# Kernel tuning notes

Measured on AMD Instinct MI355X. Metric: run time of the kernel, lower is better.

The kernel has to match this reference:

```python
import jax, jax.numpy as jnp
import numpy as np

N_NODES = 100000
N_EDGES = 3200000


def gcn_conv(x, src, dst, W, b, n):
    # x: [N, Fin] -> linear transform then symmetric-normalized scatter-add (PyG GCNConv)
    xw = x @ W  # [N, Fout]
    loop = jnp.arange(n, dtype=src.dtype)
    s = jnp.concatenate([src, loop])  # add self-loops
    d = jnp.concatenate([dst, loop])
    deg = jax.ops.segment_sum(jnp.ones_like(s, dtype=xw.dtype), d, num_segments=n)
    dinv = jnp.where(deg > 0, jax.lax.rsqrt(deg), 0.0)
    norm = dinv[s] * dinv[d]  # [E+N]
    out = jax.ops.segment_sum(xw[s] * norm[:, None], d, num_segments=n)
    return out + b


def setup_inputs() -> dict:
    key = jax.random.key(0)
    ks = jax.random.split(key, 11)
    x = jax.random.normal(ks[0], (N_NODES, 2), dtype=jnp.float32)
    edge_index = jax.random.randint(ks[1], (2, N_EDGES), 0, N_NODES, dtype=jnp.int64)
    W1 = jax.random.normal(ks[2], (2, 32), dtype=jnp.float32) * 0.5
    b1 = jax.random.normal(ks[3], (32,), dtype=jnp.float32) * 0.1
    W2 = jax.random.normal(ks[4], (32, 32), dtype=jnp.float32) * 0.18
    b2 = jax.random.normal(ks[5], (32,), dtype=jnp.float32) * 0.1
    Wf1 = jax.random.normal(ks[6], (32, 32), dtype=jnp.float32) * 0.18
    bf1 = jax.random.normal(ks[7], (32,), dtype=jnp.float32) * 0.1
    Wf2 = jax.random.normal(ks[8], (32, 1), dtype=jnp.float32) * 0.18
    bf2 = jax.random.normal(ks[9], (1,), dtype=jnp.float32) * 0.1
    return {"x": x, "edge_index": edge_index, "W1": W1, "b1": b1, "W2": W2,
            "b2": b2, "Wf1": Wf1, "bf1": bf1, "Wf2": Wf2, "bf2": bf2}


def reference(x, edge_index, W1, b1, W2, b2, Wf1, bf1, Wf2, bf2):
    n = x.shape[0]
    src, dst = edge_index[0], edge_index[1]
    h = jax.nn.relu(gcn_conv(x, src, dst, W1, b1, n))
    h = jax.nn.relu(gcn_conv(h, src, dst, W2, b2, n))
    h = jax.nn.relu(h @ Wf1 + bf1)
    return h @ Wf2 + bf2  # [N, 1]
```

## Files before the change

kernel.cpp:

```cpp
#include <hip/hip_runtime.h>

#define NGRP 512
#define CAP  6656
#define EPB  8192
#define NE   16
#define SRC_BITS 17
#define SRC_MASK 0x1FFFF

static __device__ __forceinline__ unsigned short f2bf(float f) {
    unsigned u = __float_as_uint(f);
    return (unsigned short)((u + 0x7FFFu + ((u >> 16) & 1u)) >> 16);
}
static __device__ __forceinline__ float bf2f_lo(unsigned u) { return __uint_as_float(u << 16); }
static __device__ __forceinline__ float bf2f_hi(unsigned u) { return __uint_as_float(u & 0xFFFF0000u); }


__global__ void k_init(int* gcursor) {
    gcursor[threadIdx.x] = threadIdx.x * CAP;
}

__global__ __launch_bounds__(512) void k_partition(const int* __restrict__ ei, int* gcursor,
                                                   unsigned* __restrict__ pairs,
                                                   int E, int n, int GN) {
    __shared__ int cnt[NGRP];
    __shared__ int cur[NGRP];
    int tid = threadIdx.x;
    cnt[tid] = 0;
    __syncthreads();
    int base = blockIdx.x * EPB;
    int sreg[NE], dreg[NE];
#pragma unroll
    for (int k = 0; k < NE; ++k) {
        int e = base + tid + k * 512;
        int d = -1, s = 0;
        if (e < E) {
            s = ei[e];
            d = ei[E + e];
            if ((unsigned)s < (unsigned)n && (unsigned)d < (unsigned)n)
                atomicAdd(&cnt[d / GN], 1);
            else d = -1;
        }
        sreg[k] = s; dreg[k] = d;
    }
    __syncthreads();
    { int c = cnt[tid]; cur[tid] = c ? atomicAdd(&gcursor[tid], c) : 0; }
    __syncthreads();
#pragma unroll
    for (int k = 0; k < NE; ++k) {
        int d = dreg[k];
        if (d >= 0) {
            int g = d / GN;
            int w = atomicAdd(&cur[g], 1);
            if (w < (g + 1) * CAP)
                pairs[w] = ((unsigned)(d - g * GN) << SRC_BITS) | (unsigned)sreg[k];
        }
    }
}

__global__ __launch_bounds__(512) void k_build(const int* __restrict__ gcursor,
                                               const unsigned* __restrict__ pairs,
                                               const float2* __restrict__ x2,
                                               int* __restrict__ rowStart, int* __restrict__ rowEnd,
                                               int* __restrict__ srclist, float* __restrict__ dinv,
                                               float2* __restrict__ z, int n, int GN) {
    __shared__ unsigned pl[CAP];
    __shared__ int cnt[512];
    __shared__ int cur[512];
    int g = blockIdx.x;
    int t = threadIdx.x;
    int gbeg = g * CAP;
    int gend = gcursor[g];
    int cape = gbeg + CAP;
    if (gend > cape) gend = cape;
    int m = gend - gbeg;
    cnt[t] = 0;
    __syncthreads();
    for (int k = t; k < m; k += 512) {
        unsigned v = pairs[gbeg + k];
        pl[k] = v;
        atomicAdd(&cnt[(v >> SRC_BITS) & 511], 1);
    }
    __syncthreads();
    int c = cnt[t];
    for (int off = 1; off < 512; off <<= 1) {
        int add = (t >= off) ? cnt[t - off] : 0;
        __syncthreads();
        cnt[t] += add;
        __syncthreads();
    }
    int excl = cnt[t] - c;
    int node = g * GN + t;
    if (t < GN && node < n) {
        int st = gbeg + excl;
        rowStart[node] = st;
        rowEnd[node] = st + c;
        float di = rsqrtf(1.0f + (float)c);
        dinv[node] = di;
        float2 xv = x2[node];
        z[node] = make_float2(xv.x * di, xv.y * di);
    }
    cur[t] = excl;
    __syncthreads();
    for (int k = t; k < m; k += 512) {
        unsigned v = pl[k];
        int dl = (v >> SRC_BITS) & 511;
        int pos = atomicAdd(&cur[dl], 1);
        srclist[gbeg + pos] = (int)(v & SRC_MASK);
    }
}


__global__ __launch_bounds__(256) void k_gather2f(const int* __restrict__ rowStart,
                                                  const int* __restrict__ rowEnd,
                                                  const int* __restrict__ srclist,
                                                  const float2* __restrict__ z,
                                                  float2* __restrict__ agg, int n) {
    int w = blockIdx.x * 256 + threadIdx.x;
    if (w >= n) return;
    int e = rowStart[w], end = rowEnd[w];
    float ax = 0.f, ay = 0.f;
    int s = (e < end) ? srclist[e] : 0;
    while (e < end) {
        int sc = s;
        ++e;
        if (e < end) s = srclist[e];
        float2 v = z[sc];
        ax += v.x; ay += v.y;
    }
    float2 v = z[w];
    agg[w] = make_float2(ax + v.x, ay + v.y);
}

__global__ void k_mid1(const float2* __restrict__ agg, const float* __restrict__ dinv,
                       const float* __restrict__ W1, const float* __restrict__ b1,
                       const float* __restrict__ W2, unsigned short* __restrict__ y_bf, int n) {
    __shared__ float sW[1024];
    __shared__ float sh[8][33];
    int tid = threadIdx.x;
    for (int k = tid; k < 1024; k += 256) sW[k] = W2[k];
    int ln = tid >> 5, f = tid & 31;
    int i = blockIdx.x * 8 + ln;
    float h = 0.f, di = 0.f;
    if (i < n) {
        di = dinv[i];
        float2 a = agg[i];
        h = di * (a.x * W1[f] + a.y * W1[32 + f]) + b1[f];
        h = h > 0.f ? h : 0.f;
    }
    sh[ln][f] = h;
    __syncthreads();
    if (i < n) {
        float acc = 0.f;
#pragma unroll
        for (int k = 0; k < 32; ++k) acc += sh[ln][k] * sW[k * 32 + f];
        y_bf[(size_t)i * 32 + f] = f2bf(acc * di);
    }
}

__global__ __launch_bounds__(256) void k_gather_rows(const int* __restrict__ rowStart,
                                                     const int* __restrict__ rowEnd,
                                                     const int* __restrict__ srclist,
                                                     const uint4* __restrict__ y4,
                                                     float4* __restrict__ acc4, int n) {
    int w = blockIdx.x * 64 + (threadIdx.x >> 2);
    int q = threadIdx.x & 3;
    if (w >= n) return;
    int e = rowStart[w], end = rowEnd[w];
    float a0 = 0.f, a1 = 0.f, a2 = 0.f, a3 = 0.f, a4 = 0.f, a5 = 0.f, a6 = 0.f, a7 = 0.f;
    int s = (e < end) ? srclist[e] : 0;
    while (e < end) {
        int sc = s;
        ++e;
        if (e < end) s = srclist[e];
        uint4 v = y4[(size_t)sc * 4 + q];
        a0 += bf2f_lo(v.x); a1 += bf2f_hi(v.x);
        a2 += bf2f_lo(v.y); a3 += bf2f_hi(v.y);
        a4 += bf2f_lo(v.z); a5 += bf2f_hi(v.z);
        a6 += bf2f_lo(v.w); a7 += bf2f_hi(v.w);
    }
    uint4 v = y4[(size_t)w * 4 + q];
    a0 += bf2f_lo(v.x); a1 += bf2f_hi(v.x);
    a2 += bf2f_lo(v.y); a3 += bf2f_hi(v.y);
    a4 += bf2f_lo(v.z); a5 += bf2f_hi(v.z);
    a6 += bf2f_lo(v.w); a7 += bf2f_hi(v.w);
    size_t b = (size_t)w * 8 + q * 2;
    acc4[b]     = make_float4(a0, a1, a2, a3);
    acc4[b + 1] = make_float4(a4, a5, a6, a7);
}

__global__ void k_final(const float* __restrict__ acc, const float* __restrict__ dinv,
                        const float* __restrict__ b2, const float* __restrict__ Wf1,
                        const float* __restrict__ bf1, const float* __restrict__ Wf2,
                        const float* __restrict__ bf2, float* __restrict__ out, int n) {
    __shared__ float sW[1024];
    __shared__ float sh[8][33];
    int tid = threadIdx.x;
    for (int k = tid; k < 1024; k += 256) sW[k] = Wf1[k];
    int ln = tid >> 5, f = tid & 31;
    int i = blockIdx.x * 8 + ln;
    float h = 0.f;
    if (i < n) {
        h = dinv[i] * acc[(size_t)i * 32 + f] + b2[f];
        h = h > 0.f ? h : 0.f;
    }
    sh[ln][f] = h;
    __syncthreads();
    float p = 0.f;
    if (i < n) {
        float a = bf1[f];
#pragma unroll
        for (int k = 0; k < 32; ++k) a += sh[ln][k] * sW[k * 32 + f];
        a = a > 0.f ? a : 0.f;
        p = a * Wf2[f];
    }
#pragma unroll
    for (int m = 16; m >= 1; m >>= 1) p += __shfl_xor(p, m, 64);
    if (f == 0 && i < n) out[i] = p + bf2[0];
}


extern "C" void kernel_launch(void* const* d_in, const int* in_sizes, int n_in,
                              void* d_out, int out_size, void* d_ws, size_t ws_size,
                              hipStream_t stream) {
    const float* x   = (const float*)d_in[0];
    const int*   ei  = (const int*)d_in[1];
    const float* W1  = (const float*)d_in[2];
    const float* b1  = (const float*)d_in[3];
    const float* W2  = (const float*)d_in[4];
    const float* b2  = (const float*)d_in[5];
    const float* Wf1 = (const float*)d_in[6];
    const float* bf1 = (const float*)d_in[7];
    const float* Wf2 = (const float*)d_in[8];
    const float* bf2 = (const float*)d_in[9];
    float* out = (float*)d_out;

    int n = in_sizes[0] / 2;
    int E = in_sizes[1] / 2;
    int GN = (n + NGRP - 1) / NGRP;

    float* wsf = (float*)d_ws;
    int*    srclist  = (int*)wsf;
    size_t  o = (size_t)NGRP * CAP;
    int*    rowStart = (int*)(wsf + o);     o += n;
    int*    rowEnd   = (int*)(wsf + o);     o += n;
    float*  dinv     = wsf + o;             o += n;
    float2* z        = (float2*)(wsf + o);  o += 2 * (size_t)n;
    float2* agg      = (float2*)(wsf + o);  o += 2 * (size_t)n;
    int*    gcursor  = (int*)(wsf + o);     o += NGRP;
    o = (o + 3) & ~(size_t)3;
    float*  acc      = wsf + o;             o += 32 * (size_t)n;
    unsigned short* y_bf = (unsigned short*)(wsf + o);
    unsigned* pairs = (unsigned*)acc;

    const int B = 256;
    int nblk = (E + EPB - 1) / EPB;

    k_init<<<1, NGRP, 0, stream>>>(gcursor);
    k_partition<<<nblk, 512, 0, stream>>>(ei, gcursor, pairs, E, n, GN);
    k_build<<<NGRP, 512, 0, stream>>>(gcursor, pairs, (const float2*)x, rowStart, rowEnd,
                                      srclist, dinv, z, n, GN);

    k_gather2f<<<(n + 255) / 256, B, 0, stream>>>(rowStart, rowEnd, srclist, z, agg, n);
    k_mid1<<<(n + 7) / 8, B, 0, stream>>>(agg, dinv, W1, b1, W2, y_bf, n);

    k_gather_rows<<<(n + 63) / 64, B, 0, stream>>>(rowStart, rowEnd, srclist,
                                                   (const uint4*)y_bf, (float4*)acc, n);

    k_final<<<(n + 7) / 8, B, 0, stream>>>(acc, dinv, b2, Wf1, bf1, Wf2, bf2, out, n);
}
```

Baseline: 179.8 us.

## Split layer-2 gather into two feature planes and split edges across lanes

The bf16 layer-2 features are stored as two separate 16-feature planes, each 3.2 MB rather than one 6.4 MB table, and gathered by two kernel launches so each pass's working set fits better in cache. Within a plane, each node's edge list is split between two lane pairs and the partial sums are combined with a shuffle, which gives more memory parallelism. Both gathers are also unrolled by four to issue more independent loads. In exchange, srclist and rowStart/rowEnd are read twice and there is an extra launch.

```diff
diff --git a/kernel.cpp b/kernel.cpp
--- a/kernel.cpp
+++ b/kernel.cpp
@@ -119,12 +119,14 @@
     if (w >= n) return;
     int e = rowStart[w], end = rowEnd[w];
     float ax = 0.f, ay = 0.f;
-    int s = (e < end) ? srclist[e] : 0;
-    while (e < end) {
-        int sc = s;
-        ++e;
-        if (e < end) s = srclist[e];
-        float2 v = z[sc];
+    for (; e + 4 <= end; e += 4) {
+        int s0 = srclist[e], s1 = srclist[e + 1], s2 = srclist[e + 2], s3 = srclist[e + 3];
+        float2 v0 = z[s0], v1 = z[s1], v2 = z[s2], v3 = z[s3];
+        ax += v0.x + v1.x + v2.x + v3.x;
+        ay += v0.y + v1.y + v2.y + v3.y;
+    }
+    for (; e < end; ++e) {
+        float2 v = z[srclist[e]];
         ax += v.x; ay += v.y;
     }
     float2 v = z[w];
@@ -133,7 +135,8 @@
 
 __global__ void k_mid1(const float2* __restrict__ agg, const float* __restrict__ dinv,
                        const float* __restrict__ W1, const float* __restrict__ b1,
-                       const float* __restrict__ W2, unsigned short* __restrict__ y_bf, int n) {
+                       const float* __restrict__ W2, unsigned short* __restrict__ y0,
+                       unsigned short* __restrict__ y1, int n) {
     __shared__ float sW[1024];
     __shared__ float sh[8][33];
     int tid = threadIdx.x;
@@ -153,39 +156,61 @@
         float acc = 0.f;
 #pragma unroll
         for (int k = 0; k < 32; ++k) acc += sh[ln][k] * sW[k * 32 + f];
-        y_bf[(size_t)i * 32 + f] = f2bf(acc * di);
-    }
-}
-
-__global__ __launch_bounds__(256) void k_gather_rows(const int* __restrict__ rowStart,
-                                                     const int* __restrict__ rowEnd,
-                                                     const int* __restrict__ srclist,
-                                                     const uint4* __restrict__ y4,
-                                                     float4* __restrict__ acc4, int n) {
+        unsigned short* yp = (f < 16) ? y0 : y1;
+        yp[(size_t)i * 16 + (f & 15)] = f2bf(acc * di);
+    }
+}
+
+#define ACC8(v)                                        \
+    a0 += bf2f_lo((v).x); a1 += bf2f_hi((v).x);        \
+    a2 += bf2f_lo((v).y); a3 += bf2f_hi((v).y);        \
+    a4 += bf2f_lo((v).z); a5 += bf2f_hi((v).z);        \
+    a6 += bf2f_lo((v).w); a7 += bf2f_hi((v).w);
+
+__global__ __launch_bounds__(256) void k_gather_plane(const int* __restrict__ rowStart,
+                                                      const int* __restrict__ rowEnd,
+                                                      const int* __restrict__ srclist,
+                                                      const uint4* __restrict__ yh,
+                                                      float4* __restrict__ acc4, int n, int p) {
     int w = blockIdx.x * 64 + (threadIdx.x >> 2);
-    int q = threadIdx.x & 3;
     if (w >= n) return;
-    int e = rowStart[w], end = rowEnd[w];
+    int slot = (threadIdx.x >> 1) & 1;
+    int q = threadIdx.x & 1;
+    int beg = rowStart[w], end = rowEnd[w];
+    int deg = end - beg;
+    int half = (deg + 1) >> 1;
+    int e = beg + slot * half;
+    int e1 = slot ? end : (beg + half);
     float a0 = 0.f, a1 = 0.f, a2 = 0.f, a3 = 0.f, a4 = 0.f, a5 = 0.f, a6 = 0.f, a7 = 0.f;
-    int s = (e < end) ? srclist[e] : 0;
-    while (e < end) {
-        int sc = s;
-        ++e;
-        if (e < end) s = srclist[e];
-        uint4 v = y4[(size_t)sc * 4 + q];
-        a0 += bf2f_lo(v.x); a1 += bf2f_hi(v.x);
-        a2 += bf2f_lo(v.y); a3 += bf2f_hi(v.y);
-        a4 += bf2f_lo(v.z); a5 += bf2f_hi(v.z);
-        a6 += bf2f_lo(v.w); a7 += bf2f_hi(v.w);
-    }
-    uint4 v = y4[(size_t)w * 4 + q];
-    a0 += bf2f_lo(v.x); a1 += bf2f_hi(v.x);
-    a2 += bf2f_lo(v.y); a3 += bf2f_hi(v.y);
-    a4 += bf2f_lo(v.z); a5 += bf2f_hi(v.z);
-    a6 += bf2f_lo(v.w); a7 += bf2f_hi(v.w);
-    size_t b = (size_t)w * 8 + q * 2;
-    acc4[b]     = make_float4(a0, a1, a2, a3);
-    acc4[b + 1] = make_float4(a4, a5, a6, a7);
+    for (; e + 4 <= e1; e += 4) {
+        int s0 = srclist[e], s1 = srclist[e + 1], s2 = srclist[e + 2], s3 = srclist[e + 3];
+        uint4 v0 = yh[(size_t)s0 * 2 + q];
+        uint4 v1 = yh[(size_t)s1 * 2 + q];
+        uint4 v2 = yh[(size_t)s2 * 2 + q];
+        uint4 v3 = yh[(size_t)s3 * 2 + q];
+        ACC8(v0); ACC8(v1); ACC8(v2); ACC8(v3);
+    }
+    for (; e < e1; ++e) {
+        uint4 v = yh[(size_t)srclist[e] * 2 + q];
+        ACC8(v);
+    }
+    if (slot == 0) {
+        uint4 v = yh[(size_t)w * 2 + q];
+        ACC8(v);
+    }
+    a0 += __shfl_xor(a0, 2, 64);
+    a1 += __shfl_xor(a1, 2, 64);
+    a2 += __shfl_xor(a2, 2, 64);
+    a3 += __shfl_xor(a3, 2, 64);
+    a4 += __shfl_xor(a4, 2, 64);
+    a5 += __shfl_xor(a5, 2, 64);
+    a6 += __shfl_xor(a6, 2, 64);
+    a7 += __shfl_xor(a7, 2, 64);
+    if (slot == 0) {
+        float4* dst = acc4 + (size_t)w * 8 + p * 4 + q * 2;
+        dst[0] = make_float4(a0, a1, a2, a3);
+        dst[1] = make_float4(a4, a5, a6, a7);
+    }
 }
 
 __global__ void k_final(const float* __restrict__ acc, const float* __restrict__ dinv,
@@ -249,7 +274,8 @@
     int*    gcursor  = (int*)(wsf + o);     o += NGRP;
     o = (o + 3) & ~(size_t)3;
     float*  acc      = wsf + o;             o += 32 * (size_t)n;
-    unsigned short* y_bf = (unsigned short*)(wsf + o);
+    unsigned short* y0 = (unsigned short*)(wsf + o);
+    unsigned short* y1 = y0 + (size_t)n * 16;
     unsigned* pairs = (unsigned*)acc;
 
     const int B = 256;
@@ -261,10 +287,12 @@
                                       srclist, dinv, z, n, GN);
 
     k_gather2f<<<(n + 255) / 256, B, 0, stream>>>(rowStart, rowEnd, srclist, z, agg, n);
-    k_mid1<<<(n + 7) / 8, B, 0, stream>>>(agg, dinv, W1, b1, W2, y_bf, n);
-
-    k_gather_rows<<<(n + 63) / 64, B, 0, stream>>>(rowStart, rowEnd, srclist,
-                                                   (const uint4*)y_bf, (float4*)acc, n);
+    k_mid1<<<(n + 7) / 8, B, 0, stream>>>(agg, dinv, W1, b1, W2, y0, y1, n);
+
+    k_gather_plane<<<(n + 63) / 64, B, 0, stream>>>(rowStart, rowEnd, srclist,
+                                                    (const uint4*)y0, (float4*)acc, n, 0);
+    k_gather_plane<<<(n + 63) / 64, B, 0, stream>>>(rowStart, rowEnd, srclist,
+                                                    (const uint4*)y1, (float4*)acc, n, 1);
 
     k_final<<<(n + 7) / 8, B, 0, stream>>>(acc, dinv, b2, Wf1, bf1, Wf2, bf2, out, n);
 }
```

Result: faster. 174.5 us (-2.9%).

## Replace CSR build with per-group shared-memory atomic scatter aggregation

Applied to the files above, without the earlier changes.

Drops the per-group sort into a CSR src list (rowStart/rowEnd/srclist). Degree counting and both aggregation layers now read the dst-bucketed pairs directly and accumulate into shared-memory float atomics per destination group. The second layer's 32 bf16 features are split into two 16-wide halves stored separately, each aggregated by its own launch so the shared accumulator fits. This removes the sort pass and the row-pointer indirection, but it trades register accumulation for heavy LDS atomic traffic with contention, runs only 512 blocks per launch, and adds an extra pass over the pairs.

```diff
diff --git a/kernel.cpp b/kernel.cpp
--- a/kernel.cpp
+++ b/kernel.cpp
@@ -6,6 +6,7 @@
 #define NE   16
 #define SRC_BITS 17
 #define SRC_MASK 0x1FFFF
+#define GNMAX 256
 
 static __device__ __forceinline__ unsigned short f2bf(float f) {
     unsigned u = __float_as_uint(f);
@@ -57,83 +58,60 @@
     }
 }
 
-__global__ __launch_bounds__(512) void k_build(const int* __restrict__ gcursor,
-                                               const unsigned* __restrict__ pairs,
-                                               const float2* __restrict__ x2,
-                                               int* __restrict__ rowStart, int* __restrict__ rowEnd,
-                                               int* __restrict__ srclist, float* __restrict__ dinv,
-                                               float2* __restrict__ z, int n, int GN) {
-    __shared__ unsigned pl[CAP];
+__global__ __launch_bounds__(512) void k_deg(const int* __restrict__ gcursor,
+                                             const unsigned* __restrict__ pairs,
+                                             const float2* __restrict__ x2,
+                                             float* __restrict__ dinv, float2* __restrict__ z,
+                                             int n, int GN) {
     __shared__ int cnt[512];
-    __shared__ int cur[512];
-    int g = blockIdx.x;
-    int t = threadIdx.x;
+    int g = blockIdx.x, t = threadIdx.x;
+    cnt[t] = 0;
+    __syncthreads();
     int gbeg = g * CAP;
-    int gend = gcursor[g];
-    int cape = gbeg + CAP;
-    if (gend > cape) gend = cape;
-    int m = gend - gbeg;
-    cnt[t] = 0;
-    __syncthreads();
-    for (int k = t; k < m; k += 512) {
-        unsigned v = pairs[gbeg + k];
-        pl[k] = v;
-        atomicAdd(&cnt[(v >> SRC_BITS) & 511], 1);
-    }
-    __syncthreads();
-    int c = cnt[t];
-    for (int off = 1; off < 512; off <<= 1) {
-        int add = (t >= off) ? cnt[t - off] : 0;
-        __syncthreads();
-        cnt[t] += add;
-        __syncthreads();
-    }
-    int excl = cnt[t] - c;
+    int gend = min(gcursor[g], gbeg + CAP);
+    for (int k = gbeg + t; k < gend; k += 512)
+        atomicAdd(&cnt[pairs[k] >> SRC_BITS], 1);
+    __syncthreads();
     int node = g * GN + t;
     if (t < GN && node < n) {
-        int st = gbeg + excl;
-        rowStart[node] = st;
-        rowEnd[node] = st + c;
-        float di = rsqrtf(1.0f + (float)c);
+        float di = rsqrtf(1.0f + (float)cnt[t]);
         dinv[node] = di;
         float2 xv = x2[node];
         z[node] = make_float2(xv.x * di, xv.y * di);
     }
-    cur[t] = excl;
-    __syncthreads();
-    for (int k = t; k < m; k += 512) {
-        unsigned v = pl[k];
-        int dl = (v >> SRC_BITS) & 511;
-        int pos = atomicAdd(&cur[dl], 1);
-        srclist[gbeg + pos] = (int)(v & SRC_MASK);
-    }
-}
-
-
-__global__ __launch_bounds__(256) void k_gather2f(const int* __restrict__ rowStart,
-                                                  const int* __restrict__ rowEnd,
-                                                  const int* __restrict__ srclist,
-                                                  const float2* __restrict__ z,
-                                                  float2* __restrict__ agg, int n) {
-    int w = blockIdx.x * 256 + threadIdx.x;
-    if (w >= n) return;
-    int e = rowStart[w], end = rowEnd[w];
-    float ax = 0.f, ay = 0.f;
-    int s = (e < end) ? srclist[e] : 0;
-    while (e < end) {
-        int sc = s;
-        ++e;
-        if (e < end) s = srclist[e];
-        float2 v = z[sc];
-        ax += v.x; ay += v.y;
-    }
-    float2 v = z[w];
-    agg[w] = make_float2(ax + v.x, ay + v.y);
+}
+
+
+__global__ __launch_bounds__(512) void k_gather1(const int* __restrict__ gcursor,
+                                                 const unsigned* __restrict__ pairs,
+                                                 const float2* __restrict__ z,
+                                                 float2* __restrict__ agg, int n, int GN) {
+    __shared__ float ax[512];
+    __shared__ float ay[512];
+    int g = blockIdx.x, t = threadIdx.x;
+    ax[t] = 0.f; ay[t] = 0.f;
+    __syncthreads();
+    int gbeg = g * CAP;
+    int gend = min(gcursor[g], gbeg + CAP);
+    for (int k = gbeg + t; k < gend; k += 512) {
+        unsigned v = pairs[k];
+        int dl = v >> SRC_BITS;
+        float2 zz = z[v & SRC_MASK];
+        atomicAdd(&ax[dl], zz.x);
+        atomicAdd(&ay[dl], zz.y);
+    }
+    __syncthreads();
+    int node = g * GN + t;
+    if (t < GN && node < n) {
+        float2 zz = z[node];
+        agg[node] = make_float2(ax[t] + zz.x, ay[t] + zz.y);
+    }
 }
 
 __global__ void k_mid1(const float2* __restrict__ agg, const float* __restrict__ dinv,
                        const float* __restrict__ W1, const float* __restrict__ b1,
-                       const float* __restrict__ W2, unsigned short* __restrict__ y_bf, int n) {
+                       const float* __restrict__ W2, unsigned short* __restrict__ y0,
+                       unsigned short* __restrict__ y1, int n) {
     __shared__ float sW[1024];
     __shared__ float sh[8][33];
     int tid = threadIdx.x;
@@ -153,39 +131,45 @@
         float acc = 0.f;
 #pragma unroll
         for (int k = 0; k < 32; ++k) acc += sh[ln][k] * sW[k * 32 + f];
-        y_bf[(size_t)i * 32 + f] = f2bf(acc * di);
-    }
-}
-
-__global__ __launch_bounds__(256) void k_gather_rows(const int* __restrict__ rowStart,
-                                                     const int* __restrict__ rowEnd,
-                                                     const int* __restrict__ srclist,
-                                                     const uint4* __restrict__ y4,
-                                                     float4* __restrict__ acc4, int n) {
-    int w = blockIdx.x * 64 + (threadIdx.x >> 2);
-    int q = threadIdx.x & 3;
-    if (w >= n) return;
-    int e = rowStart[w], end = rowEnd[w];
-    float a0 = 0.f, a1 = 0.f, a2 = 0.f, a3 = 0.f, a4 = 0.f, a5 = 0.f, a6 = 0.f, a7 = 0.f;
-    int s = (e < end) ? srclist[e] : 0;
-    while (e < end) {
-        int sc = s;
-        ++e;
-        if (e < end) s = srclist[e];
-        uint4 v = y4[(size_t)sc * 4 + q];
-        a0 += bf2f_lo(v.x); a1 += bf2f_hi(v.x);
-        a2 += bf2f_lo(v.y); a3 += bf2f_hi(v.y);
-        a4 += bf2f_lo(v.z); a5 += bf2f_hi(v.z);
-        a6 += bf2f_lo(v.w); a7 += bf2f_hi(v.w);
-    }
-    uint4 v = y4[(size_t)w * 4 + q];
-    a0 += bf2f_lo(v.x); a1 += bf2f_hi(v.x);
-    a2 += bf2f_lo(v.y); a3 += bf2f_hi(v.y);
-    a4 += bf2f_lo(v.z); a5 += bf2f_hi(v.z);
-    a6 += bf2f_lo(v.w); a7 += bf2f_hi(v.w);
-    size_t b = (size_t)w * 8 + q * 2;
-    acc4[b]     = make_float4(a0, a1, a2, a3);
-    acc4[b + 1] = make_float4(a4, a5, a6, a7);
+        unsigned short* yp = (f < 16) ? y0 : y1;
+        yp[(size_t)i * 16 + (f & 15)] = f2bf(acc * di);
+    }
+}
+
+__global__ __launch_bounds__(512) void k_gather2p(const int* __restrict__ gcursor,
+                                                  const unsigned* __restrict__ pairs,
+                                                  const uint4* __restrict__ yp,
+                                                  float* __restrict__ acc, int n, int GN, int p) {
+    __shared__ float pacc[GNMAX * 17];
+    int g = blockIdx.x, t = threadIdx.x;
+    for (int k = t; k < GN * 17; k += 512) pacc[k] = 0.f;
+    __syncthreads();
+    int gbeg = g * CAP;
+    int gend = min(gcursor[g], gbeg + CAP);
+    int m = gend - gbeg;
+    for (int l = t; l < 2 * m; l += 512) {
+        int e = gbeg + (l >> 1);
+        int q = l & 1;
+        unsigned v = pairs[e];
+        int dl = v >> SRC_BITS;
+        int src = v & SRC_MASK;
+        uint4 w = yp[(size_t)src * 2 + q];
+        float* b = &pacc[dl * 17 + q * 8];
+        atomicAdd(b + 0, bf2f_lo(w.x)); atomicAdd(b + 1, bf2f_hi(w.x));
+        atomicAdd(b + 2, bf2f_lo(w.y)); atomicAdd(b + 3, bf2f_hi(w.y));
+        atomicAdd(b + 4, bf2f_lo(w.z)); atomicAdd(b + 5, bf2f_hi(w.z));
+        atomicAdd(b + 6, bf2f_lo(w.w)); atomicAdd(b + 7, bf2f_hi(w.w));
+    }
+    __syncthreads();
+    const unsigned short* ys = (const unsigned short*)yp;
+    for (int k = t; k < GN * 16; k += 512) {
+        int dl = k >> 4, f = k & 15;
+        int node = g * GN + dl;
+        if (node < n) {
+            float sv = __uint_as_float((unsigned)ys[(size_t)node * 16 + f] << 16);
+            acc[(size_t)node * 32 + p * 16 + f] = pacc[dl * 17 + f] + sv;
+        }
+    }
 }
 
 __global__ void k_final(const float* __restrict__ acc, const float* __restrict__ dinv,
@@ -239,32 +223,28 @@
     int GN = (n + NGRP - 1) / NGRP;
 
     float* wsf = (float*)d_ws;
-    int*    srclist  = (int*)wsf;
+    unsigned* pairs = (unsigned*)wsf;
     size_t  o = (size_t)NGRP * CAP;
-    int*    rowStart = (int*)(wsf + o);     o += n;
-    int*    rowEnd   = (int*)(wsf + o);     o += n;
     float*  dinv     = wsf + o;             o += n;
     float2* z        = (float2*)(wsf + o);  o += 2 * (size_t)n;
     float2* agg      = (float2*)(wsf + o);  o += 2 * (size_t)n;
     int*    gcursor  = (int*)(wsf + o);     o += NGRP;
     o = (o + 3) & ~(size_t)3;
     float*  acc      = wsf + o;             o += 32 * (size_t)n;
-    unsigned short* y_bf = (unsigned short*)(wsf + o);
-    unsigned* pairs = (unsigned*)acc;
-
-    const int B = 256;
+    unsigned short* y0 = (unsigned short*)(wsf + o);
+    unsigned short* y1 = y0 + (size_t)n * 16;
+
     int nblk = (E + EPB - 1) / EPB;
 
     k_init<<<1, NGRP, 0, stream>>>(gcursor);
     k_partition<<<nblk, 512, 0, stream>>>(ei, gcursor, pairs, E, n, GN);
-    k_build<<<NGRP, 512, 0, stream>>>(gcursor, pairs, (const float2*)x, rowStart, rowEnd,
-                                      srclist, dinv, z, n, GN);
-
-    k_gather2f<<<(n + 255) / 256, B, 0, stream>>>(rowStart, rowEnd, srclist, z, agg, n);
-    k_mid1<<<(n + 7) / 8, B, 0, stream>>>(agg, dinv, W1, b1, W2, y_bf, n);
-
-    k_gather_rows<<<(n + 63) / 64, B, 0, stream>>>(rowStart, rowEnd, srclist,
-                                                   (const uint4*)y_bf, (float4*)acc, n);
-
-    k_final<<<(n + 7) / 8, B, 0, stream>>>(acc, dinv, b2, Wf1, bf1, Wf2, bf2, out, n);
-}
+    k_deg<<<NGRP, 512, 0, stream>>>(gcursor, pairs, (const float2*)x, dinv, z, n, GN);
+
+    k_gather1<<<NGRP, 512, 0, stream>>>(gcursor, pairs, z, agg, n, GN);
+    k_mid1<<<(n + 7) / 8, 256, 0, stream>>>(agg, dinv, W1, b1, W2, y0, y1, n);
+
+    k_gather2p<<<NGRP, 512, 0, stream>>>(gcursor, pairs, (const uint4*)y0, acc, n, GN, 0);
+    k_gather2p<<<NGRP, 512, 0, stream>>>(gcursor, pairs, (const uint4*)y1, acc, n, GN, 1);
+
+    k_final<<<(n + 7) / 8, 256, 0, stream>>>(acc, dinv, b2, Wf1, bf1, Wf2, bf2, out, n);
+}
```

After: 646.0 us. +259.3%, slower.
